# Performance work log

Hardware: AMD Instinct MI355X
Metric: run time of the kernel (lower is better)

The kernel has to match this reference:

```python
import jax, jax.numpy as jnp
import numpy as np

N_HEAD = 50000
N_TAIL = 50000
E = 800000
F_IN = 256
D = 64
H = 4
FE = 64
N_ETYPES = 5
NEG_SLOPE = 0.2


def setup_inputs() -> dict:
    key = jax.random.key(0)
    ks = jax.random.split(key, 10)
    head_feature = jax.random.normal(ks[0], (N_HEAD, F_IN), jnp.float32)
    tail_feature = jax.random.normal(ks[1], (N_TAIL, F_IN), jnp.float32)
    head_ind = jax.random.randint(ks[2], (E,), 0, N_HEAD)
    tail_ind = jax.random.randint(ks[3], (E,), 0, N_TAIL)
    edge_list = jnp.stack([head_ind, tail_ind], axis=0)  # [2, E]
    tmp_edge = jax.random.randint(ks[4], (E,), 0, N_ETYPES)
    s = 0.05  # small init scale, mimics uniform(-stdv, stdv)
    W = jax.random.normal(ks[5], (F_IN, D * H), jnp.float32) * s
    W_e = jax.random.normal(ks[6], (FE, FE * H), jnp.float32) * s
    edge_emb = jax.random.normal(ks[7], (N_ETYPES, FE), jnp.float32) * s
    a_l = jax.random.normal(ks[8], (1, H, D), jnp.float32) * s
    a_r = jax.random.normal(jax.random.fold_in(ks[8], 1), (1, H, D), jnp.float32) * s
    a_e = jax.random.normal(ks[9], (1, H, FE), jnp.float32) * s
    return {
        "head_feature": head_feature,
        "tail_feature": tail_feature,
        "edge_list": edge_list,
        "tmp_edge": tmp_edge,
        "W": W,
        "W_e": W_e,
        "edge_emb": edge_emb,
        "a_l": a_l,
        "a_r": a_r,
        "a_e": a_e,
    }


def _layer(head_feature, tail_feature, head_ind, tail_ind, tmp_edge,
           W, W_e, edge_emb, a_l, a_r, a_e):
    n_head = head_feature.shape[0]
    # dense projections (dropout = identity in eval)
    h_head = (head_feature @ W).reshape(-1, H, D)      # [N_h, H, D]
    h_tail = (tail_feature @ W).reshape(-1, H, D)      # [N_t, H, D]
    e = (edge_emb @ W_e).reshape(-1, H, FE)            # [T, H, FE]
    # per-edge attention logits
    h_l = (a_l * h_head).sum(-1)[head_ind]             # [E, H]
    h_r = (a_r * h_tail).sum(-1)[tail_ind]             # [E, H]
    h_e = (a_e * e).sum(-1)[tmp_edge]                  # [E, H]
    score = jax.nn.leaky_relu(h_l + h_r + h_e, NEG_SLOPE)
    # segment softmax over edges grouped by destination (head) node, per head
    m = jax.ops.segment_max(score, head_ind, num_segments=n_head)   # [N_h, H]
    ex = jnp.exp(score - m[head_ind])                               # [E, H]
    z = jax.ops.segment_sum(ex, head_ind, num_segments=n_head)      # [N_h, H]
    alpha = ex / z[head_ind]                                        # [E, H]
    # weighted aggregation: sparse-mm per head, vectorized over heads
    msg = alpha[:, :, None] * h_tail[tail_ind]                      # [E, H, D]
    out = jax.ops.segment_sum(msg, head_ind, num_segments=n_head)   # [N_h, H, D]
    out = out.reshape(n_head, H * D)
    return jax.nn.elu(out)


def reference(head_feature, tail_feature, edge_list, tmp_edge,
              W, W_e, edge_emb, a_l, a_r, a_e):
    head_ind = edge_list[0]
    tail_ind = edge_list[1]
    return _layer(head_feature, tail_feature, head_ind, tail_ind, tmp_edge,
                  W, W_e, edge_emb, a_l, a_r, a_e)
```

## Files before the change

### kernel.cpp

```cpp
#include <hip/hip_runtime.h>
#include <hip/hip_bf16.h>
#include <math.h>

#define N_HEADN 50000
#define N_TAILN 50000
#define NE      800000
#define F_IN    256
#define HH      4
#define HD      256
#define FE      64
#define N_ETYPES 5
#define NEG_SLOPE 0.2f
#define NB_SCAN ((N_HEADN + 255) / 256)
#define NB_CVT  ((N_TAILN * F_IN) / (256 * 16))
#define NB_HIST (NE / 256)
#define NB_PROJ ((N_TAILN + 63) / 64)

typedef __attribute__((ext_vector_type(8))) short bf16x8;
typedef __attribute__((ext_vector_type(4))) float f32x4;

static __device__ __forceinline__ unsigned short f2bf(float f) {
    unsigned u = __float_as_uint(f);
    return (unsigned short)((u + 0x7FFF + ((u >> 16) & 1)) >> 16);
}
static __device__ __forceinline__ float bf2f(unsigned short u) {
    return __uint_as_float((unsigned)u << 16);
}

__global__ __launch_bounds__(256) void prep_kernel(const int* __restrict__ head,
                                                   int* __restrict__ counts,
                                                   const float* __restrict__ X,
                                                   unsigned short* __restrict__ Xb,
                                                   const float* __restrict__ W,
                                                   const float* __restrict__ a_l,
                                                   const float* __restrict__ W_e,
                                                   const float* __restrict__ a_e,
                                                   const float* __restrict__ edge_emb,
                                                   float* __restrict__ waT,
                                                   float* __restrict__ heo,
                                                   short* __restrict__ Wt) {
    const int b = blockIdx.x;
    if (b < NB_HIST) {
        int e = b * 256 + threadIdx.x;
        atomicAdd(&counts[head[e]], 1);
    } else if (b < NB_HIST + NB_CVT) {
        size_t t = (size_t)(b - NB_HIST) * 256 + threadIdx.x;
        const float4* xp = (const float4*)X + t * 4;
        float4 v0 = xp[0], v1 = xp[1], v2 = xp[2], v3 = xp[3];
        bf16x8 o0, o1;
        o0[0] = (short)f2bf(v0.x); o0[1] = (short)f2bf(v0.y);
        o0[2] = (short)f2bf(v0.z); o0[3] = (short)f2bf(v0.w);
        o0[4] = (short)f2bf(v1.x); o0[5] = (short)f2bf(v1.y);
        o0[6] = (short)f2bf(v1.z); o0[7] = (short)f2bf(v1.w);
        o1[0] = (short)f2bf(v2.x); o1[1] = (short)f2bf(v2.y);
        o1[2] = (short)f2bf(v2.z); o1[3] = (short)f2bf(v2.w);
        o1[4] = (short)f2bf(v3.x); o1[5] = (short)f2bf(v3.y);
        o1[6] = (short)f2bf(v3.z); o1[7] = (short)f2bf(v3.w);
        bf16x8* op = (bf16x8*)(Xb + t * 16);
        op[0] = o0;
        op[1] = o1;
    } else if (b == NB_HIST + NB_CVT) {
        int k = threadIdx.x;
        #pragma unroll
        for (int h = 0; h < HH; ++h) {
            float s = 0.f;
            for (int d = 0; d < 64; ++d) s += a_l[h * 64 + d] * W[(size_t)k * HD + h * 64 + d];
            waT[h * 256 + k] = s;
        }
    } else if (b == NB_HIST + NB_CVT + 1) {
        __shared__ float wae[FE][HH];
        int t = threadIdx.x;
        int k = t >> 2, h = t & 3;
        float s = 0.f;
        for (int f = 0; f < 64; ++f) s += a_e[h * 64 + f] * W_e[(size_t)k * (FE * HH) + h * 64 + f];
        wae[k][h] = s;
        __syncthreads();
        if (t < N_ETYPES * HH) {
            int ty = t >> 2, hh = t & 3;
            float acc = 0.f;
            for (int kk = 0; kk < FE; ++kk) acc += edge_emb[ty * FE + kk] * wae[kk][hh];
            heo[ty * HH + hh] = acc;
        }
    } else {
        int n = b - (NB_HIST + NB_CVT + 2), k = threadIdx.x;
        Wt[(size_t)n * 256 + k] = (short)f2bf(W[(size_t)k * 256 + n]);
    }
}

__global__ void blocksum_kernel(const int* __restrict__ counts, int* __restrict__ blockSums) {
    __shared__ int s[256];
    int t = threadIdx.x, j = blockIdx.x * 256 + t;
    s[t] = (j < N_HEADN) ? counts[j] : 0;
    __syncthreads();
    for (int off = 128; off > 0; off >>= 1) {
        if (t < off) s[t] += s[t + off];
        __syncthreads();
    }
    if (t == 0) blockSums[blockIdx.x] = s[0];
}

__global__ void blockscan_kernel(const int* __restrict__ blockSums, int* __restrict__ blockOff) {
    __shared__ int s[256];
    int t = threadIdx.x;
    int v = (t < NB_SCAN) ? blockSums[t] : 0;
    s[t] = v;
    __syncthreads();
    for (int off = 1; off < 256; off <<= 1) {
        int u = (t >= off) ? s[t - off] : 0;
        __syncthreads();
        s[t] += u;
        __syncthreads();
    }
    if (t < NB_SCAN) blockOff[t] = s[t] - v;
}

__global__ void rowstart_kernel(const int* __restrict__ counts, const int* __restrict__ blockOff,
                                int* __restrict__ row_start, int* __restrict__ cursor) {
    __shared__ int s[256];
    int t = threadIdx.x, j = blockIdx.x * 256 + t;
    int c = (j < N_HEADN) ? counts[j] : 0;
    s[t] = c;
    __syncthreads();
    for (int off = 1; off < 256; off <<= 1) {
        int u = (t >= off) ? s[t - off] : 0;
        __syncthreads();
        s[t] += u;
        __syncthreads();
    }
    int excl = blockOff[blockIdx.x] + s[t] - c;
    if (j < N_HEADN) {
        row_start[j] = excl;
        cursor[j]    = excl;
        if (j == N_HEADN - 1) row_start[N_HEADN] = excl + c;
    }
}

__global__ __launch_bounds__(256) void head_dot_kernel(const float* __restrict__ X,
                                                       const float* __restrict__ waT,
                                                       float* __restrict__ hl) {
    const int wave = threadIdx.x >> 6;
    const int lane = threadIdx.x & 63;
    const int n = blockIdx.x * 4 + wave;
    float4 x = ((const float4*)(X + (size_t)n * F_IN))[lane];
    float p[HH];
    #pragma unroll
    for (int h = 0; h < HH; ++h) {
        float4 w = ((const float4*)(waT + h * 256))[lane];
        p[h] = x.x * w.x + x.y * w.y + x.z * w.z + x.w * w.w;
    }
    #pragma unroll
    for (int off = 1; off < 64; off <<= 1) {
        #pragma unroll
        for (int h = 0; h < HH; ++h) p[h] += __shfl_xor(p[h], off);
    }
    if (lane < HH) hl[(size_t)n * HH + lane] = p[lane];
}

__global__ __launch_bounds__(256) void proj_mfma_kernel(const unsigned short* __restrict__ Xb,
                                                        const short* __restrict__ Wt,
                                                        const float* __restrict__ a,
                                                        unsigned short* __restrict__ h_out,
                                                        float* __restrict__ hr,
                                                        int N) {
    const int head = blockIdx.x & 3;
    const int n0   = (blockIdx.x >> 2) * 64;
    const int wv   = threadIdx.x >> 6;
    const int lane = threadIdx.x & 63;
    const int quad = lane >> 4;
    const int l15  = lane & 15;

    __shared__ float hrbuf[4][64];

    int rbase[4];
    #pragma unroll
    for (int mt = 0; mt < 4; ++mt) {
        int r = n0 + mt * 16;
        rbase[mt] = (r + 16 <= N) ? r : (N - 16);
    }

    const short* wbase = Wt + (size_t)(head * 64 + wv * 16 + l15) * 256 + quad * 8;
    bf16x8 breg[8];
    #pragma unroll
    for (int kk = 0; kk < 8; ++kk) breg[kk] = *(const bf16x8*)(wbase + kk * 32);

    f32x4 acc[4];
    #pragma unroll
    for (int mt = 0; mt < 4; ++mt) acc[mt] = (f32x4){0.f, 0.f, 0.f, 0.f};

    const unsigned short* xrow[4];
    #pragma unroll
    for (int mt = 0; mt < 4; ++mt)
        xrow[mt] = Xb + (size_t)(rbase[mt] + l15) * F_IN + quad * 8;

    #pragma unroll
    for (int kk = 0; kk < 8; ++kk) {
        bf16x8 af[4];
        #pragma unroll
        for (int mt = 0; mt < 4; ++mt) af[mt] = *(const bf16x8*)(xrow[mt] + kk * 32);
        #pragma unroll
        for (int mt = 0; mt < 4; ++mt)
            acc[mt] = __builtin_amdgcn_mfma_f32_16x16x32_bf16(af[mt], breg[kk], acc[mt], 0, 0, 0);
    }

    const float av = a[head * 64 + wv * 16 + l15];

    #pragma unroll
    for (int mt = 0; mt < 4; ++mt) {
        #pragma unroll
        for (int r = 0; r < 4; ++r) {
            int row = rbase[mt] + quad * 4 + r;
            h_out[(size_t)row * HD + head * 64 + wv * 16 + l15] = f2bf(acc[mt][r]);
        }
        #pragma unroll
        for (int r = 0; r < 4; ++r) {
            float p = av * acc[mt][r];
            p += __shfl_xor(p, 1);
            p += __shfl_xor(p, 2);
            p += __shfl_xor(p, 4);
            p += __shfl_xor(p, 8);
            if (l15 == 0) hrbuf[wv][mt * 16 + quad * 4 + r] = p;
        }
    }
    __syncthreads();
    if (threadIdx.x < 64) {
        int row = threadIdx.x;
        int mt  = row >> 4;
        int rb  = (n0 + mt * 16 + 16 <= N) ? (n0 + mt * 16) : (N - 16);
        int g   = rb + (row & 15);
        float s = hrbuf[0][row] + hrbuf[1][row] + hrbuf[2][row] + hrbuf[3][row];
        hr[(size_t)g * HH + head] = s;
    }
}

__global__ void scatter_kernel(const int* __restrict__ head, const int* __restrict__ tail,
                               const int* __restrict__ etype,
                               const float* __restrict__ hl, const float* __restrict__ hr,
                               const float* __restrict__ he,
                               int* __restrict__ cursor, int* __restrict__ packed,
                               float* __restrict__ exE) {
    int e = blockIdx.x * 256 + threadIdx.x;
    int h0 = head[e];
    int tl = tail[e];
    int ty = etype[e];
    float4 L = *(const float4*)(hl + (size_t)h0 * HH);
    float4 R = *(const float4*)(hr + (size_t)tl * HH);
    float4 T = *(const float4*)(he + ty * HH);
    float s0 = L.x + R.x + T.x;
    float s1 = L.y + R.y + T.y;
    float s2 = L.z + R.z + T.z;
    float s3 = L.w + R.w + T.w;
    s0 = (s0 > 0.f) ? s0 : NEG_SLOPE * s0;
    s1 = (s1 > 0.f) ? s1 : NEG_SLOPE * s1;
    s2 = (s2 > 0.f) ? s2 : NEG_SLOPE * s2;
    s3 = (s3 > 0.f) ? s3 : NEG_SLOPE * s3;
    float w0 = __expf(s0), w1 = __expf(s1), w2 = __expf(s2), w3 = __expf(s3);
    int pos = atomicAdd(&cursor[h0], 1);
    packed[pos] = tl;
    *(float4*)(exE + (size_t)pos * HH) = make_float4(w0, w1, w2, w3);
}

__global__ __launch_bounds__(256) void agg_kernel(const int* __restrict__ row_start,
                                                  const int* __restrict__ packed,
                                                  const float* __restrict__ exE,
                                                  const unsigned short* __restrict__ h_tail,
                                                  float* __restrict__ out) {
    const int wave = threadIdx.x >> 6;
    const int lane = threadIdx.x & 63;
    const int n = blockIdx.x * 4 + wave;
    const int s = row_start[n];
    const int e = row_start[n + 1];
    const int g = lane >> 5;
    const int q = lane & 31;
    const int h = q >> 3;

    float acc[8];
    #pragma unroll
    for (int c = 0; c < 8; ++c) acc[c] = 0.f;
    float z = 0.f;

    for (int base = s; base < e; base += 64) {
        const int cnt = (e - base < 64) ? (e - base) : 64;
        int myidx = 0;
        if (base + lane < e) myidx = packed[base + lane];
        #pragma unroll 8
        for (int i = 0; i < cnt; i += 2) {
            const int j = i + g;
            const int tl = __shfl(myidx, j);
            if (j < cnt) {
                const float w = exE[(size_t)(base + j) * HH + h];
                uint4 u = *(const uint4*)(h_tail + (size_t)tl * HD + q * 8);
                #pragma unroll
                for (int d = 0; d < 4; ++d) {
                    unsigned uu = ((const unsigned*)&u)[d];
                    acc[2 * d]     += w * __uint_as_float(uu << 16);
                    acc[2 * d + 1] += w * __uint_as_float(uu & 0xFFFF0000u);
                }
                z += w;
            }
        }
    }

    #pragma unroll
    for (int c = 0; c < 8; ++c) acc[c] += __shfl_xor(acc[c], 32);
    z += __shfl_xor(z, 32);

    float4 o;
    if (z > 0.f) {
        o.x = acc[4 * g + 0] / z;
        o.y = acc[4 * g + 1] / z;
        o.z = acc[4 * g + 2] / z;
        o.w = acc[4 * g + 3] / z;
        o.x = (o.x > 0.f) ? o.x : expm1f(o.x);
        o.y = (o.y > 0.f) ? o.y : expm1f(o.y);
        o.z = (o.z > 0.f) ? o.z : expm1f(o.z);
        o.w = (o.w > 0.f) ? o.w : expm1f(o.w);
    } else {
        o = make_float4(0.f, 0.f, 0.f, 0.f);
    }
    ((float4*)(out + (size_t)n * HD))[q * 2 + g] = o;
}

extern "C" void kernel_launch(void* const* d_in, const int* in_sizes, int n_in,
                              void* d_out, int out_size, void* d_ws, size_t ws_size,
                              hipStream_t stream) {
    const float* head_feature = (const float*)d_in[0];
    const float* tail_feature = (const float*)d_in[1];
    const int*   edge_list    = (const int*)d_in[2];
    const int*   tmp_edge     = (const int*)d_in[3];
    const float* W            = (const float*)d_in[4];
    const float* W_e          = (const float*)d_in[5];
    const float* edge_emb     = (const float*)d_in[6];
    const float* a_l          = (const float*)d_in[7];
    const float* a_r          = (const float*)d_in[8];
    const float* a_e          = (const float*)d_in[9];
    const int* head_ind = edge_list;
    const int* tail_ind = edge_list + NE;

    char* ws = (char*)d_ws;
    unsigned short* h_tail = (unsigned short*)ws; ws += sizeof(unsigned short) * (size_t)N_TAILN * HD;
    unsigned short* Xb = (unsigned short*)ws;
    float* exE    = (float*)(void*)Xb;
    int*   packed = (int*)(void*)((char*)(void*)Xb + sizeof(float) * (size_t)NE * HH);
    ws += sizeof(unsigned short) * (size_t)N_TAILN * HD;
    short* Wt        = (short*)ws; ws += sizeof(short) * 256 * 256;
    float* hl        = (float*)ws; ws += sizeof(float) * (size_t)N_HEADN * HH;
    float* hr        = (float*)ws; ws += sizeof(float) * (size_t)N_TAILN * HH;
    float* waT       = (float*)ws; ws += sizeof(float) * HH * 256;
    float* he        = (float*)ws; ws += sizeof(float) * 32;
    int*   counts    = (int*)ws;   ws += sizeof(int) * (size_t)N_HEADN;
    int*   row_start = (int*)ws;   ws += sizeof(int) * (size_t)(N_HEADN + 4);
    int*   cursor    = (int*)ws;   ws += sizeof(int) * (size_t)N_HEADN;
    int*   blockSums = (int*)ws;   ws += sizeof(int) * 256;
    int*   blockOff  = (int*)ws;   ws += sizeof(int) * 256;

    hipMemsetAsync(counts, 0, sizeof(int) * (size_t)N_HEADN, stream);

    hipLaunchKernelGGL(prep_kernel, dim3(NB_HIST + NB_CVT + 258), dim3(256), 0, stream,
                       head_ind, counts, tail_feature, Xb,
                       W, a_l, W_e, a_e, edge_emb, waT, he, Wt);

    hipLaunchKernelGGL(blocksum_kernel, dim3(NB_SCAN), dim3(256), 0, stream,
                       counts, blockSums);
    hipLaunchKernelGGL(blockscan_kernel, dim3(1), dim3(256), 0, stream,
                       blockSums, blockOff);
    hipLaunchKernelGGL(rowstart_kernel, dim3(NB_SCAN), dim3(256), 0, stream,
                       counts, blockOff, row_start, cursor);

    hipLaunchKernelGGL(head_dot_kernel, dim3(N_HEADN / 4), dim3(256), 0, stream,
                       head_feature, waT, hl);
    hipLaunchKernelGGL(proj_mfma_kernel, dim3(NB_PROJ * 4), dim3(256), 0, stream,
                       Xb, Wt, a_r, h_tail, hr, N_TAILN);

    hipLaunchKernelGGL(scatter_kernel, dim3(NE / 256), dim3(256), 0, stream,
                       head_ind, tail_ind, tmp_edge, hl, hr, he, cursor, packed, exE);

    hipLaunchKernelGGL(agg_kernel, dim3(N_HEADN / 4), dim3(256), 0, stream,
                       row_start, packed, exE, h_tail, (float*)d_out);
}
```

Before: 383.8 us.

## Restructure projection GEMM to 16-row tiles and fold block scan into rowstart

```diff
diff --git a/kernel.cpp b/kernel.cpp
--- a/kernel.cpp
+++ b/kernel.cpp
@@ -14,7 +14,7 @@
 #define NB_SCAN ((N_HEADN + 255) / 256)
 #define NB_CVT  ((N_TAILN * F_IN) / (256 * 16))
 #define NB_HIST (NE / 256)
-#define NB_PROJ ((N_TAILN + 63) / 64)
+#define NB_PROJ (N_TAILN / 16)
 
 typedef __attribute__((ext_vector_type(8))) short bf16x8;
 typedef __attribute__((ext_vector_type(4))) float f32x4;
@@ -99,25 +99,21 @@
     if (t == 0) blockSums[blockIdx.x] = s[0];
 }
 
-__global__ void blockscan_kernel(const int* __restrict__ blockSums, int* __restrict__ blockOff) {
+__global__ void rowstart_kernel(const int* __restrict__ counts,
+                                const int* __restrict__ blockSums,
+                                int* __restrict__ row_start, int* __restrict__ cursor) {
+    __shared__ int bs[256];
     __shared__ int s[256];
-    int t = threadIdx.x;
-    int v = (t < NB_SCAN) ? blockSums[t] : 0;
-    s[t] = v;
+    int t = threadIdx.x, j = blockIdx.x * 256 + t;
+    bs[t] = (t < NB_SCAN) ? blockSums[t] : 0;
     __syncthreads();
     for (int off = 1; off < 256; off <<= 1) {
-        int u = (t >= off) ? s[t - off] : 0;
-        __syncthreads();
-        s[t] += u;
-        __syncthreads();
-    }
-    if (t < NB_SCAN) blockOff[t] = s[t] - v;
-}
-
-__global__ void rowstart_kernel(const int* __restrict__ counts, const int* __restrict__ blockOff,
-                                int* __restrict__ row_start, int* __restrict__ cursor) {
-    __shared__ int s[256];
-    int t = threadIdx.x, j = blockIdx.x * 256 + t;
+        int u = (t >= off) ? bs[t - off] : 0;
+        __syncthreads();
+        bs[t] += u;
+        __syncthreads();
+    }
+    const int blockOffV = (blockIdx.x == 0) ? 0 : bs[blockIdx.x - 1];
     int c = (j < N_HEADN) ? counts[j] : 0;
     s[t] = c;
     __syncthreads();
@@ -127,7 +123,7 @@
         s[t] += u;
         __syncthreads();
     }
-    int excl = blockOff[blockIdx.x] + s[t] - c;
+    int excl = blockOffV + s[t] - c;
     if (j < N_HEADN) {
         row_start[j] = excl;
         cursor[j]    = excl;
@@ -160,76 +156,48 @@
                                                         const short* __restrict__ Wt,
                                                         const float* __restrict__ a,
                                                         unsigned short* __restrict__ h_out,
-                                                        float* __restrict__ hr,
-                                                        int N) {
-    const int head = blockIdx.x & 3;
-    const int n0   = (blockIdx.x >> 2) * 64;
-    const int wv   = threadIdx.x >> 6;
+                                                        float* __restrict__ hr) {
+    const int h    = threadIdx.x >> 6;
     const int lane = threadIdx.x & 63;
     const int quad = lane >> 4;
     const int l15  = lane & 15;
-
-    __shared__ float hrbuf[4][64];
-
-    int rbase[4];
-    #pragma unroll
-    for (int mt = 0; mt < 4; ++mt) {
-        int r = n0 + mt * 16;
-        rbase[mt] = (r + 16 <= N) ? r : (N - 16);
-    }
-
-    const short* wbase = Wt + (size_t)(head * 64 + wv * 16 + l15) * 256 + quad * 8;
-    bf16x8 breg[8];
-    #pragma unroll
-    for (int kk = 0; kk < 8; ++kk) breg[kk] = *(const bf16x8*)(wbase + kk * 32);
+    const int r0   = blockIdx.x * 16;
+
+    const unsigned short* xbase = Xb + (size_t)(r0 + l15) * F_IN + quad * 8;
+    bf16x8 xf[8];
+    #pragma unroll
+    for (int kk = 0; kk < 8; ++kk) xf[kk] = *(const bf16x8*)(xbase + kk * 32);
 
     f32x4 acc[4];
     #pragma unroll
-    for (int mt = 0; mt < 4; ++mt) acc[mt] = (f32x4){0.f, 0.f, 0.f, 0.f};
-
-    const unsigned short* xrow[4];
-    #pragma unroll
-    for (int mt = 0; mt < 4; ++mt)
-        xrow[mt] = Xb + (size_t)(rbase[mt] + l15) * F_IN + quad * 8;
+    for (int ct = 0; ct < 4; ++ct) acc[ct] = (f32x4){0.f, 0.f, 0.f, 0.f};
+
+    const short* wbase = Wt + (size_t)(h * 64 + l15) * 256 + quad * 8;
 
     #pragma unroll
     for (int kk = 0; kk < 8; ++kk) {
-        bf16x8 af[4];
         #pragma unroll
-        for (int mt = 0; mt < 4; ++mt) af[mt] = *(const bf16x8*)(xrow[mt] + kk * 32);
-        #pragma unroll
-        for (int mt = 0; mt < 4; ++mt)
-            acc[mt] = __builtin_amdgcn_mfma_f32_16x16x32_bf16(af[mt], breg[kk], acc[mt], 0, 0, 0);
-    }
-
-    const float av = a[head * 64 + wv * 16 + l15];
-
-    #pragma unroll
-    for (int mt = 0; mt < 4; ++mt) {
-        #pragma unroll
-        for (int r = 0; r < 4; ++r) {
-            int row = rbase[mt] + quad * 4 + r;
-            h_out[(size_t)row * HD + head * 64 + wv * 16 + l15] = f2bf(acc[mt][r]);
+        for (int ct = 0; ct < 4; ++ct) {
+            bf16x8 wf = *(const bf16x8*)(wbase + (size_t)ct * 16 * 256 + kk * 32);
+            acc[ct] = __builtin_amdgcn_mfma_f32_16x16x32_bf16(wf, xf[kk], acc[ct], 0, 0, 0);
         }
-        #pragma unroll
-        for (int r = 0; r < 4; ++r) {
-            float p = av * acc[mt][r];
-            p += __shfl_xor(p, 1);
-            p += __shfl_xor(p, 2);
-            p += __shfl_xor(p, 4);
-            p += __shfl_xor(p, 8);
-            if (l15 == 0) hrbuf[wv][mt * 16 + quad * 4 + r] = p;
-        }
-    }
-    __syncthreads();
-    if (threadIdx.x < 64) {
-        int row = threadIdx.x;
-        int mt  = row >> 4;
-        int rb  = (n0 + mt * 16 + 16 <= N) ? (n0 + mt * 16) : (N - 16);
-        int g   = rb + (row & 15);
-        float s = hrbuf[0][row] + hrbuf[1][row] + hrbuf[2][row] + hrbuf[3][row];
-        hr[(size_t)g * HH + head] = s;
-    }
+    }
+
+    const int row = r0 + l15;
+    float hp = 0.f;
+    #pragma unroll
+    for (int ct = 0; ct < 4; ++ct) {
+        float4 av = *(const float4*)(a + h * 64 + ct * 16 + quad * 4);
+        hp += av.x * acc[ct][0] + av.y * acc[ct][1]
+            + av.z * acc[ct][2] + av.w * acc[ct][3];
+        ushort4 pk;
+        pk.x = f2bf(acc[ct][0]); pk.y = f2bf(acc[ct][1]);
+        pk.z = f2bf(acc[ct][2]); pk.w = f2bf(acc[ct][3]);
+        *(ushort4*)(h_out + (size_t)row * HD + h * 64 + ct * 16 + quad * 4) = pk;
+    }
+    hp += __shfl_xor(hp, 16);
+    hp += __shfl_xor(hp, 32);
+    if (lane < 16) hr[(size_t)row * HH + h] = hp;
 }
 
 __global__ void scatter_kernel(const int* __restrict__ head, const int* __restrict__ tail,
@@ -351,7 +319,6 @@
     int*   row_start = (int*)ws;   ws += sizeof(int) * (size_t)(N_HEADN + 4);
     int*   cursor    = (int*)ws;   ws += sizeof(int) * (size_t)N_HEADN;
     int*   blockSums = (int*)ws;   ws += sizeof(int) * 256;
-    int*   blockOff  = (int*)ws;   ws += sizeof(int) * 256;
 
     hipMemsetAsync(counts, 0, sizeof(int) * (size_t)N_HEADN, stream);
 
@@ -361,15 +328,13 @@
 
     hipLaunchKernelGGL(blocksum_kernel, dim3(NB_SCAN), dim3(256), 0, stream,
                        counts, blockSums);
-    hipLaunchKernelGGL(blockscan_kernel, dim3(1), dim3(256), 0, stream,
-                       blockSums, blockOff);
     hipLaunchKernelGGL(rowstart_kernel, dim3(NB_SCAN), dim3(256), 0, stream,
-                       counts, blockOff, row_start, cursor);
+                       counts, blockSums, row_start, cursor);
 
     hipLaunchKernelGGL(head_dot_kernel, dim3(N_HEADN / 4), dim3(256), 0, stream,
                        head_feature, waT, hl);
-    hipLaunchKernelGGL(proj_mfma_kernel, dim3(NB_PROJ * 4), dim3(256), 0, stream,
-                       Xb, Wt, a_r, h_tail, hr, N_TAILN);
+    hipLaunchKernelGGL(proj_mfma_kernel, dim3(NB_PROJ), dim3(256), 0, stream,
+                       Xb, Wt, a_r, h_tail, hr);
 
     hipLaunchKernelGGL(scatter_kernel, dim3(NE / 256), dim3(256), 0, stream,
                        head_ind, tail_ind, tmp_edge, hl, hr, he, cursor, packed, exE);
```

Result: no change. 379.1 us (-1.2%).
